# Kernel optimization log

Hardware: AMD Instinct MI355X
Metric: run time of the kernel (lower is better)

## Reference

```python
import jax, jax.numpy as jnp
import numpy as np

N = 20000   # nodes
E = 320000  # edges (before self loops)
T = 32768   # total tokens for BiLSTM/Transformer features
H = 4       # heads
C = 64      # emb_dim per head
NEG_SLOPE = 0.2


def gat_layer(x, W, a_src, a_dst, b, src, dst):
    # x: [N, Fin] -> h: [N, H, C]
    h = (x @ W).reshape(N, H, C)
    al = jnp.einsum('nhc,hc->nh', h, a_src)  # source attention logits
    ar = jnp.einsum('nhc,hc->nh', h, a_dst)  # target attention logits
    e = jax.nn.leaky_relu(al[src] + ar[dst], NEG_SLOPE)  # [Etot, H]
    m = jax.ops.segment_max(e, dst, num_segments=N)      # [N, H]
    ex = jnp.exp(e - m[dst])
    s = jax.ops.segment_sum(ex, dst, num_segments=N)
    alpha = ex / (s[dst] + 1e-16)                         # edge softmax per target
    msg = alpha[:, :, None] * h[src]                      # [Etot, H, C]
    out = jax.ops.segment_sum(msg, dst, num_segments=N)   # aggr='add'
    return out.reshape(N, H * C) + b


def setup_inputs() -> dict:
    key = jax.random.key(0)
    ks = jax.random.split(key, 32)
    s = 0.05
    rn = lambda k, sh, sc=1.0: jax.random.normal(k, sh, dtype=jnp.float32) * sc
    inp = {}
    inp['x'] = rn(ks[0], (N, 128))
    inp['edge_index'] = jax.random.randint(ks[1], (2, E), 0, N, dtype=jnp.int32)
    inp['batch'] = jnp.sort(jax.random.randint(ks[2], (N,), 0, 64, dtype=jnp.int32))
    inp['VOCindex'] = jnp.sort(jax.random.randint(ks[3], (N,), 0, T, dtype=jnp.int32))
    inp['BiLSTM_feature'] = rn(ks[4], (T, 128))
    inp['Transformer_feature'] = rn(ks[5], (T, 128))
    inp['W0'] = rn(ks[6], (128, H * C), s)
    inp['a_src0'] = rn(ks[7], (H, C), s)
    inp['a_dst0'] = rn(ks[8], (H, C), s)
    inp['b0'] = rn(ks[9], (H * C,), s)
    inp['W1'] = rn(ks[10], (H * C, H * C), s)
    inp['a_src1'] = rn(ks[11], (H, C), s)
    inp['a_dst1'] = rn(ks[12], (H, C), s)
    inp['b1'] = rn(ks[13], (H * C,), s)
    inp['W2'] = rn(ks[14], (H * C, H * C), s)
    inp['a_src2'] = rn(ks[15], (H, C), s)
    inp['a_dst2'] = rn(ks[16], (H, C), s)
    inp['b2'] = rn(ks[17], (H * C,), s)
    inp['fcmax_w'] = rn(ks[18], (H * C, H * C), s)
    inp['fcmax_b'] = rn(ks[19], (H * C,), s)
    inp['fc1_w'] = rn(ks[20], (3 * 2 * H * C, 2 * H * C), s)
    inp['fc1_b'] = rn(ks[21], (2 * H * C,), s)
    inp['fc2_w'] = rn(ks[22], (2 * H * C, 2 * C), s)
    inp['fc2_b'] = rn(ks[23], (2 * C,), s)
    inp['fc3_w'] = rn(ks[24], (2 * C, C), s)
    inp['fc3_b'] = rn(ks[25], (C,), s)
    return inp


def reference(x, edge_index, batch, VOCindex, BiLSTM_feature, Transformer_feature,
              W0, a_src0, a_dst0, b0, W1, a_src1, a_dst1, b1, W2, a_src2, a_dst2, b2,
              fcmax_w, fcmax_b, fc1_w, fc1_b, fc2_w, fc2_b, fc3_w, fc3_b):
    loop = jnp.arange(N, dtype=edge_index.dtype)
    src = jnp.concatenate([edge_index[0], loop])  # PyG GATConv adds self-loops
    dst = jnp.concatenate([edge_index[1], loop])
    params = [(W0, a_src0, a_dst0, b0), (W1, a_src1, a_dst1, b1), (W2, a_src2, a_dst2, b2)]
    h = x
    x_all = []
    for (W, asr, ads, b) in params:
        h = gat_layer(h, W, asr, ads, b, src, dst)
        x_all.append(h)
        h = jax.nn.relu(h @ fcmax_w + fcmax_b)
        x_all.append(h)
    z = jnp.concatenate(x_all, axis=1)               # [N, 1536]
    z = jax.nn.relu(z @ fc1_w + fc1_b)
    z = jax.nn.relu(z @ fc2_w + fc2_b)
    gnn_feature = z @ fc3_w + fc3_b                   # [N, C]
    b_sel = BiLSTM_feature[VOCindex]                  # [N, 128]
    t_sel = Transformer_feature[VOCindex]             # [N, 128]
    return (b_sel, t_sel, gnn_feature, batch)
```

## Files before the change

### kernel.cpp

```cpp
#include <hip/hip_runtime.h>
#include <math.h>

#define NN 20000
#define NPAD 20096
#define EE 320000
#define ET (EE + NN)

typedef __attribute__((ext_vector_type(8))) short bf16x8;
typedef __attribute__((ext_vector_type(4))) float f32x4;
typedef __attribute__((ext_vector_type(4))) unsigned short us4;
typedef __attribute__((ext_vector_type(8))) unsigned short us8;
typedef __attribute__((ext_vector_type(4))) float fx4;

__device__ inline unsigned short f2bf(float f) {
    union { float f; unsigned u; } x; x.f = f;
    unsigned u = x.u;
    return (unsigned short)((u + 0x7FFF + ((u >> 16) & 1)) >> 16);
}
__device__ inline float bf2f(unsigned short u) {
    union { unsigned u; float f; } x; x.u = (unsigned)u << 16; return x.f;
}

__device__ inline void storeC(float* C, size_t idx, float v) { C[idx] = v; }
__device__ inline void storeC(unsigned short* C, size_t idx, float v) { C[idx] = f2bf(v); }

__device__ inline void gload_lds16(const void* g, void* l) {
    __builtin_amdgcn_global_load_lds(
        (const __attribute__((address_space(1))) unsigned int*)g,
        (__attribute__((address_space(3))) unsigned int*)l, 16, 0, 0);
}

__device__ inline int xcd_swz(int orig, int nwg) {
    int q = nwg >> 3, r = nwg & 7;
    int xcd = orig & 7, loc = orig >> 3;
    return (xcd < r ? xcd * (q + 1) : r * (q + 1) + (xcd - r) * q) + loc;
}

__device__ inline void transpose_tile(const float* __restrict__ W, unsigned short* __restrict__ Wt,
                                      int K, int N, int lb) {
    __shared__ float t[32][33];
    int kb = K >> 5;
    int k0 = (lb % kb) * 32, n0 = (lb / kb) * 32;
    int c = threadIdx.x & 31, r8 = threadIdx.x >> 5;
    #pragma unroll
    for (int i = 0; i < 4; i++)
        t[r8 + i * 8][c] = W[(size_t)(k0 + r8 + i * 8) * N + n0 + c];
    __syncthreads();
    #pragma unroll
    for (int i = 0; i < 4; i++)
        Wt[(size_t)(n0 + r8 + i * 8) * K + k0 + c] = f2bf(t[c][r8 + i * 8]);
}

__global__ __launch_bounds__(256) void transpose_all(
    const float* s0, unsigned short* d0,
    const float* s1, unsigned short* d1,
    const float* s2, unsigned short* d2,
    const float* s3, unsigned short* d3,
    const float* s4, unsigned short* d4,
    const float* s5, unsigned short* d5,
    const float* s6, unsigned short* d6)
{
    int b = blockIdx.x;
    if      (b < 32)   transpose_tile(s0, d0, 128, 256, b);
    else if (b < 96)   transpose_tile(s1, d1, 256, 256, b - 32);
    else if (b < 160)  transpose_tile(s2, d2, 256, 256, b - 96);
    else if (b < 224)  transpose_tile(s3, d3, 256, 256, b - 160);
    else if (b < 992)  transpose_tile(s4, d4, 1536, 512, b - 224);
    else if (b < 1056) transpose_tile(s5, d5, 512, 128, b - 992);
    else               transpose_tile(s6, d6, 128, 64, b - 1056);
}

__global__ void cvt_bf16_v4(const float* __restrict__ in, unsigned short* __restrict__ out, int n4) {
    int i = blockIdx.x * blockDim.x + threadIdx.x;
    if (i < n4) {
        fx4 v = *(const fx4*)(in + (size_t)i * 4);
        us4 s;
        #pragma unroll
        for (int j = 0; j < 4; j++) s[j] = f2bf(v[j]);
        *(us4*)(out + (size_t)i * 4) = s;
    }
}

__global__ void count_edges(const int* dst, int* cnt) {
    int e = blockIdx.x * blockDim.x + threadIdx.x;
    if (e < EE) atomicAdd(&cnt[dst[e]], 1);
}

__global__ void scan_kernel(const int* cnt, int* indptr, int* cursor, int* esrc) {
    __shared__ int part[1024];
    int tid = threadIdx.x;
    const int CH = 20;
    int base = tid * CH;
    int sum = 0;
    for (int i = 0; i < CH; i++) {
        int idx = base + i;
        if (idx < NN) sum += cnt[idx] + 1;
    }
    part[tid] = sum;
    __syncthreads();
    for (int off = 1; off < 1024; off <<= 1) {
        int v = (tid >= off) ? part[tid - off] : 0;
        __syncthreads();
        part[tid] += v;
        __syncthreads();
    }
    int run = (tid == 0) ? 0 : part[tid - 1];
    for (int i = 0; i < CH; i++) {
        int idx = base + i;
        if (idx < NN) {
            indptr[idx] = run;
            esrc[run] = idx;
            cursor[idx] = run + 1;
            run += cnt[idx] + 1;
        }
    }
    if (tid == 1023) indptr[NN] = run;
}

__global__ void scatter_edges(const int* src, const int* dst, int* cursor, int* esrc) {
    int e = blockIdx.x * blockDim.x + threadIdx.x;
    if (e < EE) {
        int pos = atomicAdd(&cursor[dst[e]], 1);
        esrc[pos] = src[e];
    }
}

template <int KTOT, typename TC>
__global__ __launch_bounds__(256) void sshot_gemm(
    const unsigned short* __restrict__ A, int lda,
    const unsigned short* __restrict__ Bt, int ldbt,
    TC* __restrict__ C, int ldc,
    int M, const float* __restrict__ bias, int relu, int nwgx)
{
    constexpr int LPR = KTOT / 8;
    constexpr int RPC = 512 / KTOT;
    constexpr int NCH = KTOT / 8;
    constexpr int NCHW = NCH / 4;
    constexpr int KC = KTOT / 32;
    __shared__ unsigned short Als[64 * KTOT];
    __shared__ unsigned short Bls[64 * KTOT];

    int swz = xcd_swz(blockIdx.x, gridDim.x);
    int bx = swz % nwgx, by = swz / nwgx;
    int row0 = by * 64, col0 = bx * 64;

    int tid = threadIdx.x;
    int lane = tid & 63, w = tid >> 6;
    int ric = lane / LPR, slot = lane % LPR;

    #pragma unroll
    for (int i = 0; i < NCHW; i++) {
        int ch = w * NCHW + i;
        int r = ch * RPC + ric;
        gload_lds16(A + (size_t)(row0 + r) * lda + ((slot ^ (r & 7)) << 3),
                    &Als[ch * 512 + lane * 8]);
    }
    #pragma unroll
    for (int i = 0; i < NCHW; i++) {
        int ch = w * NCHW + i;
        int r = ch * RPC + ric;
        gload_lds16(Bt + (size_t)(col0 + r) * ldbt + ((slot ^ (r & 7)) << 3),
                    &Bls[ch * 512 + lane * 8]);
    }
    __syncthreads();

    f32x4 acc[4];
    #pragma unroll
    for (int j = 0; j < 4; j++) acc[j] = (f32x4){0.f, 0.f, 0.f, 0.f};

    #pragma unroll
    for (int kc = 0; kc < KC; kc++) {
        int ks = (kc << 2) + (lane >> 4);
        int ra = (w << 4) + (lane & 15);
        bf16x8 af = *(bf16x8*)&Als[ra * KTOT + ((ks ^ (ra & 7)) << 3)];
        #pragma unroll
        for (int j = 0; j < 4; j++) {
            int rb = (j << 4) + (lane & 15);
            bf16x8 bf = *(bf16x8*)&Bls[rb * KTOT + ((ks ^ (rb & 7)) << 3)];
            acc[j] = __builtin_amdgcn_mfma_f32_16x16x32_bf16(af, bf, acc[j], 0, 0, 0);
        }
    }

    #pragma unroll
    for (int rr = 0; rr < 4; rr++) {
        int row = row0 + (w << 4) + ((lane >> 4) << 2) + rr;
        if (row >= M) continue;
        #pragma unroll
        for (int j = 0; j < 4; j++) {
            int col = col0 + j * 16 + (lane & 15);
            float v = acc[j][rr] + (bias ? bias[col] : 0.f);
            if (relu) v = fmaxf(v, 0.f);
            storeC(C, (size_t)row * ldc + col, v);
        }
    }
}

__global__ __launch_bounds__(256) void mfma_gemm32(
    const unsigned short* __restrict__ A, int lda,
    const unsigned short* __restrict__ Bt, int ldbt,
    unsigned short* __restrict__ C, int ldc,
    int M, int K, const float* __restrict__ bias, int nwgx)
{
    __shared__ unsigned short Als[2][128 * 32];
    __shared__ unsigned short Bls[2][128 * 32];

    int swz = xcd_swz(blockIdx.x, gridDim.x);
    int bx = swz % nwgx, by = swz / nwgx;
    int tid = threadIdx.x, lane = tid & 63, w = tid >> 6;
    int wm = w >> 1, wn = w & 1;
    int row0 = by * 128, col0 = bx * 128;

    int ric = lane >> 2;
    int scol = ((lane & 3) ^ ((ric >> 1) & 3)) << 3;

    f32x4 acc[4][4];
    #pragma unroll
    for (int i = 0; i < 4; i++)
        #pragma unroll
        for (int j = 0; j < 4; j++) acc[i][j] = (f32x4){0.f, 0.f, 0.f, 0.f};

    auto stage = [&](int buf, int k0) {
        #pragma unroll
        for (int i = 0; i < 2; i++) {
            int ch = w * 2 + i;
            int r = (ch << 4) + ric;
            gload_lds16(A + (size_t)(row0 + r) * lda + k0 + scol,
                        &Als[buf][(ch << 9) + (lane << 3)]);
        }
        #pragma unroll
        for (int i = 0; i < 2; i++) {
            int ch = w * 2 + i;
            int r = (ch << 4) + ric;
            gload_lds16(Bt + (size_t)(col0 + r) * ldbt + k0 + scol,
                        &Bls[buf][(ch << 9) + (lane << 3)]);
        }
    };

    auto compute = [&](int buf) {
        int ks = lane >> 4;
        bf16x8 af[4], bfr[4];
        #pragma unroll
        for (int i = 0; i < 4; i++) {
            int rr = wm * 64 + (i << 4) + (lane & 15);
            af[i] = *(bf16x8*)&Als[buf][(rr << 5) + ((ks ^ ((rr >> 1) & 3)) << 3)];
        }
        #pragma unroll
        for (int j = 0; j < 4; j++) {
            int rr = wn * 64 + (j << 4) + (lane & 15);
            bfr[j] = *(bf16x8*)&Bls[buf][(rr << 5) + ((ks ^ ((rr >> 1) & 3)) << 3)];
        }
        #pragma unroll
        for (int i = 0; i < 4; i++)
            #pragma unroll
            for (int j = 0; j < 4; j++)
                acc[i][j] = __builtin_amdgcn_mfma_f32_16x16x32_bf16(af[i], bfr[j], acc[i][j], 0, 0, 0);
    };

    int NT = K >> 5;
    stage(0, 0);
    stage(1, 32);
    for (int t = 0; t < NT; ++t) {
        if (t < NT - 1)
            asm volatile("s_waitcnt vmcnt(4)" ::: "memory");
        else
            asm volatile("s_waitcnt vmcnt(0)" ::: "memory");
        __builtin_amdgcn_s_barrier();
        compute(t & 1);
        if (t + 2 < NT) {
            __builtin_amdgcn_s_barrier();
            stage(t & 1, (t + 2) << 5);
        }
    }

    #pragma unroll
    for (int i = 0; i < 4; i++) {
        #pragma unroll
        for (int rr = 0; rr < 4; rr++) {
            int row = row0 + wm * 64 + (i << 4) + ((lane >> 4) << 2) + rr;
            if (row >= M) continue;
            #pragma unroll
            for (int j = 0; j < 4; j++) {
                int col = col0 + wn * 64 + j * 16 + (lane & 15);
                float v = fmaxf(acc[i][j][rr] + bias[col], 0.f);
                C[(size_t)row * ldc + col] = f2bf(v);
            }
        }
    }
}

template <int BN, typename TC, bool LOGITS>
__global__ __launch_bounds__(256) void mfma_gemm(
    const unsigned short* __restrict__ A, int lda,
    const unsigned short* __restrict__ Bt, int ldbt,
    TC* __restrict__ C, int ldc,
    int M, int K,
    const float* __restrict__ bias, int relu, int nwgx,
    const float* __restrict__ asrc, const float* __restrict__ adst,
    float* __restrict__ al, float* __restrict__ ar)
{
    constexpr int BM = 128, BK = 64;
    constexpr int WNW = (BN >= 128) ? 2 : 1;
    constexpr int WMW = 4 / WNW;
    constexpr int RW = BM / WMW;
    constexpr int NI = RW / 16;
    constexpr int NJ = 4;
    constexpr int NCHB = BN / 8;
    constexpr int PER_STAGE = 4 + NCHB / 4;
    __shared__ unsigned short Als[2][BM * BK];
    __shared__ unsigned short Bls[2][BN * BK];

    int swz = xcd_swz(blockIdx.x, gridDim.x);
    int bx = swz % nwgx, by = swz / nwgx;

    int tid = threadIdx.x;
    int lane = tid & 63, w = tid >> 6;
    int wm = (WNW == 2) ? (w >> 1) : w;
    int wn = (WNW == 2) ? (w & 1) : 0;
    int row0 = by * BM, col0 = bx * BN;

    int lr = lane >> 3;
    int scol = ((lane & 7) ^ lr) << 3;

    f32x4 acc[NI][NJ];
    #pragma unroll
    for (int i = 0; i < NI; i++)
        #pragma unroll
        for (int j = 0; j < NJ; j++) acc[i][j] = (f32x4){0.f, 0.f, 0.f, 0.f};

    auto stage = [&](int buf, int k0) {
        #pragma unroll
        for (int i = 0; i < 4; i++) {
            int ch = (w << 2) + i;
            gload_lds16(A + (size_t)(row0 + (ch << 3) + lr) * lda + k0 + scol,
                        &Als[buf][(ch << 9) + (lane << 3)]);
        }
        #pragma unroll
        for (int i = 0; i < NCHB / 4; i++) {
            int ch = w * (NCHB / 4) + i;
            gload_lds16(Bt + (size_t)(col0 + (ch << 3) + lr) * ldbt + k0 + scol,
                        &Bls[buf][(ch << 9) + (lane << 3)]);
        }
    };

    auto compute = [&](int buf) {
        #pragma unroll
        for (int kc = 0; kc < 2; kc++) {
            int ks = (kc << 2) + (lane >> 4);
            bf16x8 af[NI];
            #pragma unroll
            for (int i = 0; i < NI; i++) {
                int rr = wm * RW + (i << 4) + (lane & 15);
                af[i] = *(bf16x8*)&Als[buf][(rr << 6) + ((ks ^ (rr & 7)) << 3)];
            }
            bf16x8 bfr[NJ];
            #pragma unroll
            for (int j = 0; j < NJ; j++) {
                int rr = wn * 64 + (j << 4) + (lane & 15);
                bfr[j] = *(bf16x8*)&Bls[buf][(rr << 6) + ((ks ^ (rr & 7)) << 3)];
            }
            #pragma unroll
            for (int i = 0; i < NI; i++)
                #pragma unroll
                for (int j = 0; j < NJ; j++)
                    acc[i][j] = __builtin_amdgcn_mfma_f32_16x16x32_bf16(af[i], bfr[j], acc[i][j], 0, 0, 0);
        }
    };

    int NT = K >> 6;
    stage(0, 0);
    stage(1, BK);
    for (int t = 0; t < NT; ++t) {
        if (t < NT - 1)
            asm volatile("s_waitcnt vmcnt(%0)" :: "i"(PER_STAGE) : "memory");
        else
            asm volatile("s_waitcnt vmcnt(0)" ::: "memory");
        __builtin_amdgcn_s_barrier();
        compute(t & 1);
        if (t + 2 < NT) {
            __builtin_amdgcn_s_barrier();
            stage(t & 1, (t + 2) << 6);
        }
    }

    if constexpr (LOGITS) {
        int hh = col0 >> 6;
        float as_j[NJ], ad_j[NJ];
        #pragma unroll
        for (int j = 0; j < NJ; j++) {
            int cl = j * 16 + (lane & 15);
            as_j[j] = asrc[hh * 64 + cl];
            ad_j[j] = adst[hh * 64 + cl];
        }
        #pragma unroll
        for (int i = 0; i < NI; i++) {
            #pragma unroll
            for (int rr = 0; rr < 4; rr++) {
                int row = row0 + wm * RW + (i << 4) + ((lane >> 4) << 2) + rr;
                float ps = 0.f, pd = 0.f;
                #pragma unroll
                for (int j = 0; j < NJ; j++) {
                    float v = acc[i][j][rr];
                    ps += v * as_j[j];
                    pd += v * ad_j[j];
                    if (row < M) {
                        int col = col0 + j * 16 + (lane & 15);
                        storeC(C, (size_t)row * ldc + col, v);
                    }
                }
                #pragma unroll
                for (int off = 8; off; off >>= 1) {
                    ps += __shfl_xor(ps, off);
                    pd += __shfl_xor(pd, off);
                }
                if ((lane & 15) == 0 && row < M) {
                    al[row * 4 + hh] = ps;
                    ar[row * 4 + hh] = pd;
                }
            }
        }
    } else {
        #pragma unroll
        for (int i = 0; i < NI; i++) {
            #pragma unroll
            for (int rr = 0; rr < 4; rr++) {
                int row = row0 + wm * RW + (i << 4) + ((lane >> 4) << 2) + rr;
                if (row >= M) continue;
                #pragma unroll
                for (int j = 0; j < NJ; j++) {
                    int col = col0 + wn * 64 + j * 16 + (lane & 15);
                    float v = acc[i][j][rr] + (bias ? bias[col] : 0.f);
                    if (relu) v = fmaxf(v, 0.f);
                    storeC(C, (size_t)row * ldc + col, v);
                }
            }
        }
    }
}

__global__ __launch_bounds__(256) void aggregate_kernel(
    const unsigned short* __restrict__ hbuf,
    const float* __restrict__ al, const float* __restrict__ ar,
    const int* __restrict__ indptr, const int* __restrict__ esrc,
    const float* __restrict__ bias,
    unsigned short* __restrict__ out, int ldo)
{
    int w = threadIdx.x >> 6;
    int n = blockIdx.x * 4 + w;
    if (n >= NN) return;
    int lane = threadIdx.x & 63;
    int myh = lane >> 4;
    int c4 = lane * 4;
    int beg = indptr[n], end = indptr[n + 1];

    float arh = ar[(size_t)n * 4 + myh];

    float ssum = 0.f;
    fx4 acc = (fx4){0.f, 0.f, 0.f, 0.f};
    int j = beg;
    for (; j + 4 <= end; j += 4) {
        int s0 = esrc[j], s1 = esrc[j + 1], s2 = esrc[j + 2], s3 = esrc[j + 3];
        us4 h0 = *(const us4*)&hbuf[(size_t)s0 * 256 + c4];
        us4 h1 = *(const us4*)&hbuf[(size_t)s1 * 256 + c4];
        us4 h2 = *(const us4*)&hbuf[(size_t)s2 * 256 + c4];
        us4 h3 = *(const us4*)&hbuf[(size_t)s3 * 256 + c4];
        float a0 = al[(size_t)s0 * 4 + myh];
        float a1 = al[(size_t)s1 * 4 + myh];
        float a2 = al[(size_t)s2 * 4 + myh];
        float a3 = al[(size_t)s3 * 4 + myh];
        float e0 = a0 + arh; e0 = e0 > 0.f ? e0 : 0.2f * e0;
        float e1 = a1 + arh; e1 = e1 > 0.f ? e1 : 0.2f * e1;
        float e2 = a2 + arh; e2 = e2 > 0.f ? e2 : 0.2f * e2;
        float e3 = a3 + arh; e3 = e3 > 0.f ? e3 : 0.2f * e3;
        float x0 = __expf(e0), x1 = __expf(e1);
        float x2 = __expf(e2), x3 = __expf(e3);
        ssum += x0 + x1 + x2 + x3;
        #pragma unroll
        for (int k = 0; k < 4; k++)
            acc[k] += x0 * bf2f(h0[k]) + x1 * bf2f(h1[k])
                    + x2 * bf2f(h2[k]) + x3 * bf2f(h3[k]);
    }
    for (; j < end; j++) {
        int s = esrc[j];
        us4 hv = *(const us4*)&hbuf[(size_t)s * 256 + c4];
        float a = al[(size_t)s * 4 + myh];
        float e = a + arh; e = e > 0.f ? e : 0.2f * e;
        float ex = __expf(e);
        ssum += ex;
        #pragma unroll
        for (int k = 0; k < 4; k++) acc[k] += ex * bf2f(hv[k]);
    }

    float inv = 1.f / (ssum + 1e-16f);
    us4 o;
    #pragma unroll
    for (int k = 0; k < 4; k++) o[k] = f2bf(acc[k] * inv + bias[c4 + k]);
    *(us4*)&out[(size_t)n * ldo + c4] = o;
}

__global__ void gather_feats(const float* __restrict__ Bf, const float* __restrict__ Tf,
                             const int* __restrict__ voc, const int* __restrict__ batch,
                             float* __restrict__ out)
{
    int i = blockIdx.x * blockDim.x + threadIdx.x;
    if (i < NN * 32) {
        int n = i >> 5, c4 = (i & 31) * 4;
        int t = voc[n];
        *(fx4*)&out[(size_t)n * 128 + c4] = *(const fx4*)&Bf[(size_t)t * 128 + c4];
        *(fx4*)&out[(size_t)NN * 128 + (size_t)n * 128 + c4] = *(const fx4*)&Tf[(size_t)t * 128 + c4];
    }
    if (i < NN) out[(size_t)NN * 128 * 2 + (size_t)NN * 64 + i] = (float)batch[i];
}

extern "C" void kernel_launch(void* const* d_in, const int* in_sizes, int n_in,
                              void* d_out, int out_size, void* d_ws, size_t ws_size,
                              hipStream_t stream) {
    const float* x     = (const float*)d_in[0];
    const int*   ei    = (const int*)d_in[1];
    const int*   batch = (const int*)d_in[2];
    const int*   voc   = (const int*)d_in[3];
    const float* Bf    = (const float*)d_in[4];
    const float* Tf    = (const float*)d_in[5];
    const float* W0    = (const float*)d_in[6];
    const float* as0   = (const float*)d_in[7];
    const float* ad0   = (const float*)d_in[8];
    const float* b0    = (const float*)d_in[9];
    const float* W1    = (const float*)d_in[10];
    const float* as1   = (const float*)d_in[11];
    const float* ad1   = (const float*)d_in[12];
    const float* b1    = (const float*)d_in[13];
    const float* W2    = (const float*)d_in[14];
    const float* as2   = (const float*)d_in[15];
    const float* ad2   = (const float*)d_in[16];
    const float* b2    = (const float*)d_in[17];
    const float* fcmax_w = (const float*)d_in[18];
    const float* fcmax_b = (const float*)d_in[19];
    const float* fc1_w = (const float*)d_in[20];
    const float* fc1_b = (const float*)d_in[21];
    const float* fc2_w = (const float*)d_in[22];
    const float* fc2_b = (const float*)d_in[23];
    const float* fc3_w = (const float*)d_in[24];
    const float* fc3_b = (const float*)d_in[25];
    float* out = (float*)d_out;

    char* p = (char*)d_ws;
    unsigned short* xb  = (unsigned short*)p; p += (size_t)NPAD * 128 * 2;
    unsigned short* hbuf= (unsigned short*)p; p += (size_t)NN * 256 * 2;
    unsigned short* z   = (unsigned short*)p; p += (size_t)NPAD * 1536 * 2;
    unsigned short* z1  = (unsigned short*)p; p += (size_t)NPAD * 512 * 2;
    unsigned short* h2  = (unsigned short*)p; p += (size_t)NPAD * 128 * 2;
    unsigned short* w0t = (unsigned short*)p; p += (size_t)128 * 256 * 2;
    unsigned short* w1t = (unsigned short*)p; p += (size_t)256 * 256 * 2;
    unsigned short* w2t = (unsigned short*)p; p += (size_t)256 * 256 * 2;
    unsigned short* wmt = (unsigned short*)p; p += (size_t)256 * 256 * 2;
    unsigned short* f1t = (unsigned short*)p; p += (size_t)1536 * 512 * 2;
    unsigned short* f2t = (unsigned short*)p; p += (size_t)512 * 128 * 2;
    unsigned short* f3t = (unsigned short*)p; p += (size_t)128 * 64 * 2;
    float* al   = (float*)p; p += (size_t)NN * 4 * 4;
    float* ar   = (float*)p; p += (size_t)NN * 4 * 4;
    int* cnt    = (int*)p;   p += (size_t)NN * 4;
    int* cursor = (int*)p;   p += (size_t)NN * 4;
    int* esrc   = (int*)p;   p += (size_t)ET * 4;
    int* indptr = (int*)p;   p += (size_t)(NN + 1) * 4;

    const int* e_src = ei;
    const int* e_dst = ei + EE;

    transpose_all<<<1064, 256, 0, stream>>>(W0, w0t, W1, w1t, W2, w2t, fcmax_w, wmt,
                                            fc1_w, f1t, fc2_w, f2t, fc3_w, f3t);
    cvt_bf16_v4<<<(NN * 32 + 255) / 256, 256, 0, stream>>>(x, xb, NN * 32);

    hipMemsetAsync(cnt, 0, (size_t)NN * 4, stream);
    count_edges<<<(EE + 255) / 256, 256, 0, stream>>>(e_dst, cnt);
    scan_kernel<<<1, 1024, 0, stream>>>(cnt, indptr, cursor, esrc);
    scatter_edges<<<(EE + 255) / 256, 256, 0, stream>>>(e_src, e_dst, cursor, esrc);

    gather_feats<<<(NN * 32 + 255) / 256, 256, 0, stream>>>(Bf, Tf, voc, batch, out);

    const int MB = NPAD / 128;
    const int SB = NPAD / 64;
    const int NB4 = (NN + 3) / 4;

    mfma_gemm<64, unsigned short, true><<<4 * MB, 256, 0, stream>>>(xb, 128, w0t, 128, hbuf, 256, NN, 128, nullptr, 0, 4, as0, ad0, al, ar);
    aggregate_kernel<<<NB4, 256, 0, stream>>>(hbuf, al, ar, indptr, esrc, b0, z + 0, 1536);
    mfma_gemm<64, unsigned short, false><<<4 * MB, 256, 0, stream>>>(z + 0, 1536, wmt, 256, z + 256, 1536, NN, 256, fcmax_b, 1, 4, nullptr, nullptr, nullptr, nullptr);

    mfma_gemm<64, unsigned short, true><<<4 * MB, 256, 0, stream>>>(z + 256, 1536, w1t, 256, hbuf, 256, NN, 256, nullptr, 0, 4, as1, ad1, al, ar);
    aggregate_kernel<<<NB4, 256, 0, stream>>>(hbuf, al, ar, indptr, esrc, b1, z + 512, 1536);
    mfma_gemm<64, unsigned short, false><<<4 * MB, 256, 0, stream>>>(z + 512, 1536, wmt, 256, z + 768, 1536, NN, 256, fcmax_b, 1, 4, nullptr, nullptr, nullptr, nullptr);

    mfma_gemm<64, unsigned short, true><<<4 * MB, 256, 0, stream>>>(z + 768, 1536, w2t, 256, hbuf, 256, NN, 256, nullptr, 0, 4, as2, ad2, al, ar);
    aggregate_kernel<<<NB4, 256, 0, stream>>>(hbuf, al, ar, indptr, esrc, b2, z + 1024, 1536);
    mfma_gemm<64, unsigned short, false><<<4 * MB, 256, 0, stream>>>(z + 1024, 1536, wmt, 256, z + 1280, 1536, NN, 256, fcmax_b, 1, 4, nullptr, nullptr, nullptr, nullptr);

    mfma_gemm32<<<4 * MB, 256, 0, stream>>>(z, 1536, f1t, 1536, z1, 512, NN, 1536, fc1_b, 4);
    mfma_gemm<64, unsigned short, false><<<2 * MB, 256, 0, stream>>>(z1, 512, f2t, 512, h2, 128, NN, 512, fc2_b, 1, 2, nullptr, nullptr, nullptr, nullptr);
    sshot_gemm<128, float><<<1 * SB, 256, 0, stream>>>(h2, 128, f3t, 128, out + (size_t)2 * NN * 128, 64, NN, fc3_b, 0, 1);
}
```

Measured before the change: 316.9 us.

## Shrink GEMM row tiles, widen aggregate vectors, fold x conversion into transpose

```diff
diff --git a/kernel.cpp b/kernel.cpp
--- a/kernel.cpp
+++ b/kernel.cpp
@@ -58,7 +58,8 @@
     const float* s3, unsigned short* d3,
     const float* s4, unsigned short* d4,
     const float* s5, unsigned short* d5,
-    const float* s6, unsigned short* d6)
+    const float* s6, unsigned short* d6,
+    const float* xf, unsigned short* xb)
 {
     int b = blockIdx.x;
     if      (b < 32)   transpose_tile(s0, d0, 128, 256, b);
@@ -67,17 +68,16 @@
     else if (b < 224)  transpose_tile(s3, d3, 256, 256, b - 160);
     else if (b < 992)  transpose_tile(s4, d4, 1536, 512, b - 224);
     else if (b < 1056) transpose_tile(s5, d5, 512, 128, b - 992);
-    else               transpose_tile(s6, d6, 128, 64, b - 1056);
-}
-
-__global__ void cvt_bf16_v4(const float* __restrict__ in, unsigned short* __restrict__ out, int n4) {
-    int i = blockIdx.x * blockDim.x + threadIdx.x;
-    if (i < n4) {
-        fx4 v = *(const fx4*)(in + (size_t)i * 4);
-        us4 s;
-        #pragma unroll
-        for (int j = 0; j < 4; j++) s[j] = f2bf(v[j]);
-        *(us4*)(out + (size_t)i * 4) = s;
+    else if (b < 1064) transpose_tile(s6, d6, 128, 64, b - 1056);
+    else {
+        int i = (b - 1064) * 256 + threadIdx.x;
+        if (i < NN * 32) {
+            fx4 v = *(const fx4*)(xf + (size_t)i * 4);
+            us4 s;
+            #pragma unroll
+            for (int j = 0; j < 4; j++) s[j] = f2bf(v[j]);
+            *(us4*)(xb + (size_t)i * 4) = s;
+        }
     }
 }
 
@@ -288,7 +288,7 @@
     }
 }
 
-template <int BN, typename TC, bool LOGITS>
+template <int BM, int BN, typename TC, bool LOGITS>
 __global__ __launch_bounds__(256) void mfma_gemm(
     const unsigned short* __restrict__ A, int lda,
     const unsigned short* __restrict__ Bt, int ldbt,
@@ -298,14 +298,13 @@
     const float* __restrict__ asrc, const float* __restrict__ adst,
     float* __restrict__ al, float* __restrict__ ar)
 {
-    constexpr int BM = 128, BK = 64;
-    constexpr int WNW = (BN >= 128) ? 2 : 1;
-    constexpr int WMW = 4 / WNW;
-    constexpr int RW = BM / WMW;
+    constexpr int BK = 64;
+    constexpr int RW = BM / 4;
     constexpr int NI = RW / 16;
     constexpr int NJ = 4;
+    constexpr int NCHA = BM / 8;
     constexpr int NCHB = BN / 8;
-    constexpr int PER_STAGE = 4 + NCHB / 4;
+    constexpr int PER_STAGE = NCHA / 4 + NCHB / 4;
     __shared__ unsigned short Als[2][BM * BK];
     __shared__ unsigned short Bls[2][BN * BK];
 
@@ -314,8 +313,6 @@
 
     int tid = threadIdx.x;
     int lane = tid & 63, w = tid >> 6;
-    int wm = (WNW == 2) ? (w >> 1) : w;
-    int wn = (WNW == 2) ? (w & 1) : 0;
     int row0 = by * BM, col0 = bx * BN;
 
     int lr = lane >> 3;
@@ -329,8 +326,8 @@
 
     auto stage = [&](int buf, int k0) {
         #pragma unroll
-        for (int i = 0; i < 4; i++) {
-            int ch = (w << 2) + i;
+        for (int i = 0; i < NCHA / 4; i++) {
+            int ch = w * (NCHA / 4) + i;
             gload_lds16(A + (size_t)(row0 + (ch << 3) + lr) * lda + k0 + scol,
                         &Als[buf][(ch << 9) + (lane << 3)]);
         }
@@ -349,13 +346,13 @@
             bf16x8 af[NI];
             #pragma unroll
             for (int i = 0; i < NI; i++) {
-                int rr = wm * RW + (i << 4) + (lane & 15);
+                int rr = w * RW + (i << 4) + (lane & 15);
                 af[i] = *(bf16x8*)&Als[buf][(rr << 6) + ((ks ^ (rr & 7)) << 3)];
             }
             bf16x8 bfr[NJ];
             #pragma unroll
             for (int j = 0; j < NJ; j++) {
-                int rr = wn * 64 + (j << 4) + (lane & 15);
+                int rr = (j << 4) + (lane & 15);
                 bfr[j] = *(bf16x8*)&Bls[buf][(rr << 6) + ((ks ^ (rr & 7)) << 3)];
             }
             #pragma unroll
@@ -395,7 +392,7 @@
         for (int i = 0; i < NI; i++) {
             #pragma unroll
             for (int rr = 0; rr < 4; rr++) {
-                int row = row0 + wm * RW + (i << 4) + ((lane >> 4) << 2) + rr;
+                int row = row0 + w * RW + (i << 4) + ((lane >> 4) << 2) + rr;
                 float ps = 0.f, pd = 0.f;
                 #pragma unroll
                 for (int j = 0; j < NJ; j++) {
@@ -423,11 +420,11 @@
         for (int i = 0; i < NI; i++) {
             #pragma unroll
             for (int rr = 0; rr < 4; rr++) {
-                int row = row0 + wm * RW + (i << 4) + ((lane >> 4) << 2) + rr;
+                int row = row0 + w * RW + (i << 4) + ((lane >> 4) << 2) + rr;
                 if (row >= M) continue;
                 #pragma unroll
                 for (int j = 0; j < NJ; j++) {
-                    int col = col0 + wn * 64 + j * 16 + (lane & 15);
+                    int col = col0 + j * 16 + (lane & 15);
                     float v = acc[i][j][rr] + (bias ? bias[col] : 0.f);
                     if (relu) v = fmaxf(v, 0.f);
                     storeC(C, (size_t)row * ldc + col, v);
@@ -444,25 +441,25 @@
     const float* __restrict__ bias,
     unsigned short* __restrict__ out, int ldo)
 {
-    int w = threadIdx.x >> 6;
-    int n = blockIdx.x * 4 + w;
+    int sub = threadIdx.x >> 5;
+    int n = blockIdx.x * 8 + sub;
     if (n >= NN) return;
-    int lane = threadIdx.x & 63;
-    int myh = lane >> 4;
-    int c4 = lane * 4;
+    int lane = threadIdx.x & 31;
+    int myh = lane >> 3;
+    int c8 = lane * 8;
     int beg = indptr[n], end = indptr[n + 1];
 
     float arh = ar[(size_t)n * 4 + myh];
 
     float ssum = 0.f;
-    fx4 acc = (fx4){0.f, 0.f, 0.f, 0.f};
+    float acc[8] = {};
     int j = beg;
     for (; j + 4 <= end; j += 4) {
         int s0 = esrc[j], s1 = esrc[j + 1], s2 = esrc[j + 2], s3 = esrc[j + 3];
-        us4 h0 = *(const us4*)&hbuf[(size_t)s0 * 256 + c4];
-        us4 h1 = *(const us4*)&hbuf[(size_t)s1 * 256 + c4];
-        us4 h2 = *(const us4*)&hbuf[(size_t)s2 * 256 + c4];
-        us4 h3 = *(const us4*)&hbuf[(size_t)s3 * 256 + c4];
+        us8 h0 = *(const us8*)&hbuf[(size_t)s0 * 256 + c8];
+        us8 h1 = *(const us8*)&hbuf[(size_t)s1 * 256 + c8];
+        us8 h2 = *(const us8*)&hbuf[(size_t)s2 * 256 + c8];
+        us8 h3 = *(const us8*)&hbuf[(size_t)s3 * 256 + c8];
         float a0 = al[(size_t)s0 * 4 + myh];
         float a1 = al[(size_t)s1 * 4 + myh];
         float a2 = al[(size_t)s2 * 4 + myh];
@@ -475,26 +472,26 @@
         float x2 = __expf(e2), x3 = __expf(e3);
         ssum += x0 + x1 + x2 + x3;
         #pragma unroll
-        for (int k = 0; k < 4; k++)
+        for (int k = 0; k < 8; k++)
             acc[k] += x0 * bf2f(h0[k]) + x1 * bf2f(h1[k])
                     + x2 * bf2f(h2[k]) + x3 * bf2f(h3[k]);
     }
     for (; j < end; j++) {
         int s = esrc[j];
-        us4 hv = *(const us4*)&hbuf[(size_t)s * 256 + c4];
+        us8 hv = *(const us8*)&hbuf[(size_t)s * 256 + c8];
         float a = al[(size_t)s * 4 + myh];
         float e = a + arh; e = e > 0.f ? e : 0.2f * e;
         float ex = __expf(e);
         ssum += ex;
         #pragma unroll
-        for (int k = 0; k < 4; k++) acc[k] += ex * bf2f(hv[k]);
+        for (int k = 0; k < 8; k++) acc[k] += ex * bf2f(hv[k]);
     }
 
     float inv = 1.f / (ssum + 1e-16f);
-    us4 o;
-    #pragma unroll
-    for (int k = 0; k < 4; k++) o[k] = f2bf(acc[k] * inv + bias[c4 + k]);
-    *(us4*)&out[(size_t)n * ldo + c4] = o;
+    us8 o;
+    #pragma unroll
+    for (int k = 0; k < 8; k++) o[k] = f2bf(acc[k] * inv + bias[c8 + k]);
+    *(us8*)&out[(size_t)n * ldo + c8] = o;
 }
 
 __global__ void gather_feats(const float* __restrict__ Bf, const float* __restrict__ Tf,
@@ -565,9 +562,8 @@
     const int* e_src = ei;
     const int* e_dst = ei + EE;
 
-    transpose_all<<<1064, 256, 0, stream>>>(W0, w0t, W1, w1t, W2, w2t, fcmax_w, wmt,
-                                            fc1_w, f1t, fc2_w, f2t, fc3_w, f3t);
-    cvt_bf16_v4<<<(NN * 32 + 255) / 256, 256, 0, stream>>>(x, xb, NN * 32);
+    transpose_all<<<1064 + 2500, 256, 0, stream>>>(W0, w0t, W1, w1t, W2, w2t, fcmax_w, wmt,
+                                                   fc1_w, f1t, fc2_w, f2t, fc3_w, f3t, x, xb);
 
     hipMemsetAsync(cnt, 0, (size_t)NN * 4, stream);
     count_edges<<<(EE + 255) / 256, 256, 0, stream>>>(e_dst, cnt);
@@ -578,21 +574,21 @@
 
     const int MB = NPAD / 128;
     const int SB = NPAD / 64;
-    const int NB4 = (NN + 3) / 4;
-
-    mfma_gemm<64, unsigned short, true><<<4 * MB, 256, 0, stream>>>(xb, 128, w0t, 128, hbuf, 256, NN, 128, nullptr, 0, 4, as0, ad0, al, ar);
-    aggregate_kernel<<<NB4, 256, 0, stream>>>(hbuf, al, ar, indptr, esrc, b0, z + 0, 1536);
-    mfma_gemm<64, unsigned short, false><<<4 * MB, 256, 0, stream>>>(z + 0, 1536, wmt, 256, z + 256, 1536, NN, 256, fcmax_b, 1, 4, nullptr, nullptr, nullptr, nullptr);
-
-    mfma_gemm<64, unsigned short, true><<<4 * MB, 256, 0, stream>>>(z + 256, 1536, w1t, 256, hbuf, 256, NN, 256, nullptr, 0, 4, as1, ad1, al, ar);
-    aggregate_kernel<<<NB4, 256, 0, stream>>>(hbuf, al, ar, indptr, esrc, b1, z + 512, 1536);
-    mfma_gemm<64, unsigned short, false><<<4 * MB, 256, 0, stream>>>(z + 512, 1536, wmt, 256, z + 768, 1536, NN, 256, fcmax_b, 1, 4, nullptr, nullptr, nullptr, nullptr);
-
-    mfma_gemm<64, unsigned short, true><<<4 * MB, 256, 0, stream>>>(z + 768, 1536, w2t, 256, hbuf, 256, NN, 256, nullptr, 0, 4, as2, ad2, al, ar);
-    aggregate_kernel<<<NB4, 256, 0, stream>>>(hbuf, al, ar, indptr, esrc, b2, z + 1024, 1536);
-    mfma_gemm<64, unsigned short, false><<<4 * MB, 256, 0, stream>>>(z + 1024, 1536, wmt, 256, z + 1280, 1536, NN, 256, fcmax_b, 1, 4, nullptr, nullptr, nullptr, nullptr);
+    const int NB8 = (NN + 7) / 8;
+
+    mfma_gemm<64, 64, unsigned short, true><<<4 * SB, 256, 0, stream>>>(xb, 128, w0t, 128, hbuf, 256, NN, 128, nullptr, 0, 4, as0, ad0, al, ar);
+    aggregate_kernel<<<NB8, 256, 0, stream>>>(hbuf, al, ar, indptr, esrc, b0, z + 0, 1536);
+    mfma_gemm<64, 64, unsigned short, false><<<4 * SB, 256, 0, stream>>>(z + 0, 1536, wmt, 256, z + 256, 1536, NN, 256, fcmax_b, 1, 4, nullptr, nullptr, nullptr, nullptr);
+
+    mfma_gemm<64, 64, unsigned short, true><<<4 * SB, 256, 0, stream>>>(z + 256, 1536, w1t, 256, hbuf, 256, NN, 256, nullptr, 0, 4, as1, ad1, al, ar);
+    aggregate_kernel<<<NB8, 256, 0, stream>>>(hbuf, al, ar, indptr, esrc, b1, z + 512, 1536);
+    mfma_gemm<64, 64, unsigned short, false><<<4 * SB, 256, 0, stream>>>(z + 512, 1536, wmt, 256, z + 768, 1536, NN, 256, fcmax_b, 1, 4, nullptr, nullptr, nullptr, nullptr);
+
+    mfma_gemm<64, 64, unsigned short, true><<<4 * SB, 256, 0, stream>>>(z + 768, 1536, w2t, 256, hbuf, 256, NN, 256, nullptr, 0, 4, as2, ad2, al, ar);
+    aggregate_kernel<<<NB8, 256, 0, stream>>>(hbuf, al, ar, indptr, esrc, b2, z + 1024, 1536);
+    mfma_gemm<64, 64, unsigned short, false><<<4 * SB, 256, 0, stream>>>(z + 1024, 1536, wmt, 256, z + 1280, 1536, NN, 256, fcmax_b, 1, 4, nullptr, nullptr, nullptr, nullptr);
 
     mfma_gemm32<<<4 * MB, 256, 0, stream>>>(z, 1536, f1t, 1536, z1, 512, NN, 1536, fc1_b, 4);
-    mfma_gemm<64, unsigned short, false><<<2 * MB, 256, 0, stream>>>(z1, 512, f2t, 512, h2, 128, NN, 512, fc2_b, 1, 2, nullptr, nullptr, nullptr, nullptr);
+    mfma_gemm<64, 64, unsigned short, false><<<2 * SB, 256, 0, stream>>>(z1, 512, f2t, 512, h2, 128, NN, 512, fc2_b, 1, 2, nullptr, nullptr, nullptr, nullptr);
     sshot_gemm<128, float><<<1 * SB, 256, 0, stream>>>(h2, 128, f3t, 128, out + (size_t)2 * NN * 128, 64, NN, fc3_b, 0, 1);
 }
```

Measured after the change: 307.2 us. 1.03x faster.
